# Performance work log

Measured on AMD Instinct MI355X. Metric: run time of the kernel, lower is better.

Reference implementation:

```python
import jax, jax.numpy as jnp
import numpy as np

B, N, F, C, L = 2, 2048, 64, 64, 4

def setup_inputs() -> dict:
    key = jax.random.key(0)
    k1, k2, k3, k4, k5 = jax.random.split(key, 5)
    V = jax.random.normal(k1, (B, N, F), dtype=jnp.float32)
    A = jax.random.uniform(k2, (B, N, N, L), dtype=jnp.float32)
    # xavier-normal-ish scale for w1; plain normals for w2/w3
    w1 = jax.random.normal(k3, (F, C), dtype=jnp.float32) * jnp.sqrt(2.0 / (F + C))
    w2 = jax.random.normal(k4, (F * L, C), dtype=jnp.float32) * 0.05
    w3 = jax.random.normal(k5, (F * L, C), dtype=jnp.float32) * 0.05
    return {"V": V, "A": A, "w1": w1, "w2": w2, "w3": w3}

def reference(V, A, w1, w2, w3):
    b, n, _, l = A.shape
    f = V.shape[-1]
    # term1: plain linear embedding (no bias, no act)
    term1 = jnp.matmul(V, w1)                                   # B,N,C
    # term2: per-edge-type degree weighting of self features
    deg = jnp.sum(A, axis=2)                                    # B,N,L  (sum over neighbors j)
    dv = (deg[..., None] * V[:, :, None, :]).reshape(b, n, l * f)  # B,N,L*F
    term2 = jnp.matmul(dv, w2)                                  # B,N,C
    # term3: neighbor aggregation per edge type
    agg = jnp.einsum('bijl,bjf->bilf', A, V).reshape(b, n, l * f)  # B,N,L*F
    term3 = jnp.matmul(agg, w3)                                 # B,N,C
    return jax.nn.sigmoid(term1 + term2 - term3)
```

## Files before the change

kernel.cpp:

```cpp
#include <hip/hip_runtime.h>

#define B_ 2
#define N_ 2048
#define F_ 64
#define C_ 64
#define L_ 4
#define SK 4
#define NJ (N_ / SK)
#define TSTEPS (NJ / 32)
#define PJ 40

typedef _Float16 half8 __attribute__((ext_vector_type(8)));
typedef _Float16 half2 __attribute__((ext_vector_type(2)));
typedef float floatx4 __attribute__((ext_vector_type(4)));

__global__ __launch_bounds__(256) void k0_transpose(const float* __restrict__ V,
                                                    _Float16* __restrict__ Vth) {
    __shared__ float tile[64][65];
    const int b  = blockIdx.x >> 5;
    const int j0 = (blockIdx.x & 31) * 64;
    const int tid = threadIdx.x;

    const floatx4* V4 = (const floatx4*)(V + ((size_t)(b * N_ + j0)) * F_);
#pragma unroll
    for (int s = 0; s < 4; ++s) {
        int g = tid + 256 * s;
        int jl = g >> 4;
        int fq = g & 15;
        floatx4 v = V4[jl * 16 + fq];
        tile[jl][fq * 4 + 0] = v.x;
        tile[jl][fq * 4 + 1] = v.y;
        tile[jl][fq * 4 + 2] = v.z;
        tile[jl][fq * 4 + 3] = v.w;
    }
    __syncthreads();

    const int f = tid >> 2;
    const int jb = (tid & 3) * 16;
    _Float16* dh = Vth + ((size_t)(b * F_ + f)) * N_ + j0 + jb;
#pragma unroll
    for (int u = 0; u < 16; u += 4) {
        half2 h01 = {(_Float16)tile[jb + u + 0][f], (_Float16)tile[jb + u + 1][f]};
        half2 h23 = {(_Float16)tile[jb + u + 2][f], (_Float16)tile[jb + u + 3][f]};
        *(half2*)(dh + u + 0) = h01;
        *(half2*)(dh + u + 2) = h23;
    }
}

__global__ __launch_bounds__(256, 4) void k1_agg(const float* __restrict__ A,
                                                 const _Float16* __restrict__ Vth,
                                                 float* __restrict__ aggT,
                                                 float* __restrict__ degT) {
    __shared__ _Float16 lds[2 * 4 * 16 * PJ];

    const int bid = blockIdx.x;
    const int b   = bid >> 9;
    const int rem = bid & 511;
    const int i0  = (rem >> 2) * 16;
    const int p   = rem & 3;
    const int tid  = threadIdx.x;
    const int w    = tid >> 6;
    const int lane = tid & 63;
    const int m    = lane & 15;
    const int q    = lane >> 4;

    const int i_s = tid >> 4;
    const int jp  = tid & 15;

    const floatx4* Abase = (const floatx4*)A + ((size_t)(b * N_ + i0 + i_s)) * N_ + p * NJ;
    const _Float16* Vrow = Vth + ((size_t)b * F_) * N_ + p * NJ;

    floatx4 acc0 = {0,0,0,0}, acc1 = {0,0,0,0}, acc2 = {0,0,0,0}, acc3 = {0,0,0,0};
    floatx4 accd = {0,0,0,0};

    half8 bones;
#pragma unroll
    for (int e = 0; e < 8; ++e) bones[e] = (m == 0) ? (_Float16)1.0f : (_Float16)0.0f;

    floatx4 a_cur0, a_cur1, a_nxt0, a_nxt1;
    half8 v_cur0, v_cur1, v_cur2, v_cur3, v_nxt0, v_nxt1, v_nxt2, v_nxt3;

#define LOAD_A(t, x0, x1) do { int jj = (t) * 32 + 2 * jp; x0 = Abase[jj]; x1 = Abase[jj + 1]; } while (0)
#define LOAD_V(t, v0, v1, v2, v3) do { int jj = (t) * 32 + q * 8;                                  \
        v0 = *(const half8*)(Vrow + (size_t)(0  + m) * N_ + jj);                                   \
        v1 = *(const half8*)(Vrow + (size_t)(16 + m) * N_ + jj);                                   \
        v2 = *(const half8*)(Vrow + (size_t)(32 + m) * N_ + jj);                                   \
        v3 = *(const half8*)(Vrow + (size_t)(48 + m) * N_ + jj); } while (0)

    LOAD_A(0, a_cur0, a_cur1);
    LOAD_V(0, v_cur0, v_cur1, v_cur2, v_cur3);
    LOAD_A(1, a_nxt0, a_nxt1);
    LOAD_V(1, v_nxt0, v_nxt1, v_nxt2, v_nxt3);

#pragma unroll 2
    for (int t = 0; t < TSTEPS; ++t) {
        const int buf = t & 1;
        _Float16* dst = lds + buf * (4 * 16 * PJ);
        {
            const float* c0 = (const float*)&a_cur0;
            const float* c1 = (const float*)&a_cur1;
#pragma unroll
            for (int l = 0; l < 4; ++l) {
                half2 h = {(_Float16)c0[l], (_Float16)c1[l]};
                *(half2*)(dst + (l * 16 + i_s) * PJ + 2 * jp) = h;
            }
        }
        __syncthreads();

        a_cur0 = a_nxt0; a_cur1 = a_nxt1;
        const int tn = (t + 2 < TSTEPS) ? (t + 2) : (TSTEPS - 1);
        LOAD_A(tn, a_nxt0, a_nxt1);

        half8 af = *(const half8*)(lds + buf * (4 * 16 * PJ) + (w * 16 + m) * PJ + q * 8);
        acc0 = __builtin_amdgcn_mfma_f32_16x16x32_f16(af, v_cur0, acc0, 0, 0, 0);
        acc1 = __builtin_amdgcn_mfma_f32_16x16x32_f16(af, v_cur1, acc1, 0, 0, 0);
        acc2 = __builtin_amdgcn_mfma_f32_16x16x32_f16(af, v_cur2, acc2, 0, 0, 0);
        acc3 = __builtin_amdgcn_mfma_f32_16x16x32_f16(af, v_cur3, acc3, 0, 0, 0);
        accd = __builtin_amdgcn_mfma_f32_16x16x32_f16(af, bones,  accd, 0, 0, 0);

        v_cur0 = v_nxt0; v_cur1 = v_nxt1; v_cur2 = v_nxt2; v_cur3 = v_nxt3;
        LOAD_V(tn, v_nxt0, v_nxt1, v_nxt2, v_nxt3);
    }
#undef LOAD_A
#undef LOAD_V

    float* aggb = aggT + ((size_t)(p * B_ + b)) * 256 * N_;
    const int ibase = i0 + q * 4;
    {
        int k = w * 64 + 0  + m; *(floatx4*)(aggb + (size_t)k * N_ + ibase) = acc0;
    }
    {
        int k = w * 64 + 16 + m; *(floatx4*)(aggb + (size_t)k * N_ + ibase) = acc1;
    }
    {
        int k = w * 64 + 32 + m; *(floatx4*)(aggb + (size_t)k * N_ + ibase) = acc2;
    }
    {
        int k = w * 64 + 48 + m; *(floatx4*)(aggb + (size_t)k * N_ + ibase) = acc3;
    }
    if (m == 0) {
        *(floatx4*)(degT + ((size_t)((p * B_ + b) * L_ + w)) * N_ + ibase) = accd;
    }
}

__global__ __launch_bounds__(256) void k2_out(const float* __restrict__ V,
                                              const float* __restrict__ degT,
                                              const float* __restrict__ aggT,
                                              const float* __restrict__ w1,
                                              const float* __restrict__ w2,
                                              const float* __restrict__ w3,
                                              float* __restrict__ out) {
    __shared__ float xsum[256][4];
    __shared__ float vt[4][64];
    __shared__ float dsum[4][4];

    const int raw = blockIdx.x;
    const int b   = raw >> 9;
    const int t9  = raw & 511;
    const int tile = ((t9 & 7) << 6) | (t9 >> 3);
    const int i0  = tile * 4;
    const int tid = threadIdx.x;

    {
        const int k = tid;
        const float* g = aggT + ((size_t)b * 256 + k) * N_ + i0;
        const size_t PS = (size_t)B_ * 256 * N_;
        floatx4 s = *(const floatx4*)(g);
        s += *(const floatx4*)(g + PS);
        s += *(const floatx4*)(g + 2 * PS);
        s += *(const floatx4*)(g + 3 * PS);
        *(floatx4*)&xsum[k][0] = s;
    }
    {
        const int il = tid >> 6, f = tid & 63;
        vt[il][f] = V[((size_t)(b * N_ + i0 + il)) * F_ + f];
    }
    if (tid < 16) {
        const int l = tid >> 2, il = tid & 3;
        float s = 0.0f;
#pragma unroll
        for (int p = 0; p < SK; ++p)
            s += degT[((size_t)((p * B_ + b) * L_ + l)) * N_ + i0 + il];
        dsum[l][il] = s;
    }
    __syncthreads();

    const int il = tid >> 6;
    const int c  = tid & 63;
    const float d0 = dsum[0][il], d1 = dsum[1][il], d2 = dsum[2][il], d3 = dsum[3][il];

    float acc = 0.0f;
#pragma unroll 4
    for (int f = 0; f < 64; ++f) {
        const float x = vt[il][f];
        acc += x        * w1[f * 64 + c];
        acc += (d0 * x) * w2[(0 * 64 + f) * 64 + c];
        acc += (d1 * x) * w2[(1 * 64 + f) * 64 + c];
        acc += (d2 * x) * w2[(2 * 64 + f) * 64 + c];
        acc += (d3 * x) * w2[(3 * 64 + f) * 64 + c];
    }
#pragma unroll 4
    for (int k = 0; k < 256; ++k) {
        acc -= xsum[k][il] * w3[k * 64 + c];
    }

    out[((size_t)(b * N_ + i0 + il)) * C_ + c] = 1.0f / (1.0f + __expf(-acc));
}

extern "C" void kernel_launch(void* const* d_in, const int* in_sizes, int n_in,
                              void* d_out, int out_size, void* d_ws, size_t ws_size,
                              hipStream_t stream) {
    const float* V  = (const float*)d_in[0];
    const float* A  = (const float*)d_in[1];
    const float* w1 = (const float*)d_in[2];
    const float* w2 = (const float*)d_in[3];
    const float* w3 = (const float*)d_in[4];
    float* out = (float*)d_out;

    char* ws = (char*)d_ws;
    float*    aggT = (float*)(ws);
    float*    degT = (float*)(ws + 16777216);
    _Float16* Vth  = (_Float16*)(ws + 17039360);

    hipLaunchKernelGGL(k0_transpose, dim3(B_ * (N_ / 64)), dim3(256), 0, stream, V, Vth);
    hipLaunchKernelGGL(k1_agg,       dim3(B_ * (N_ / 16) * SK), dim3(256), 0, stream,
                       A, Vth, aggT, degT);
    hipLaunchKernelGGL(k2_out,       dim3(B_ * (N_ / 4)), dim3(256), 0, stream,
                       V, degT, aggT, w1, w2, w3, out);
}
```

Baseline: 244.6 us.

## Reassociate weight projections before neighbor aggregation and reduce partials in-block

Precomputes U3 = V·w3 per edge type (fp16), U2 = V·w2 and T1 = V·w1 in the first kernel, so the A-aggregation multiplies A directly against projected features. The per-type results are summed across the four waves in LDS, so only a 64-wide partial per row goes out instead of the 256-wide aggT. This cuts workspace traffic and simplifies the final kernel to an elementwise combine plus sigmoid. The main A-streaming kernel keeps the same MFMA work, and the __syncthreads is swapped for an explicit waitcnt plus s_barrier. Holding U3 in fp16 may change rounding compared with holding V in fp16.

```diff
diff --git a/kernel.cpp b/kernel.cpp
--- a/kernel.cpp
+++ b/kernel.cpp
@@ -1,4 +1,5 @@
 #include <hip/hip_runtime.h>
+
 
 #define B_ 2
 #define N_ 2048
@@ -14,44 +15,70 @@
 typedef _Float16 half2 __attribute__((ext_vector_type(2)));
 typedef float floatx4 __attribute__((ext_vector_type(4)));
 
-__global__ __launch_bounds__(256) void k0_transpose(const float* __restrict__ V,
-                                                    _Float16* __restrict__ Vth) {
-    __shared__ float tile[64][65];
-    const int b  = blockIdx.x >> 5;
-    const int j0 = (blockIdx.x & 31) * 64;
+__global__ __launch_bounds__(256) void k0_embed(const float* __restrict__ V,
+                                                const float* __restrict__ w1,
+                                                const float* __restrict__ w2,
+                                                const float* __restrict__ w3,
+                                                _Float16* __restrict__ U3,
+                                                float* __restrict__ U2,
+                                                float* __restrict__ T1) {
+    __shared__ float vt[16][64];
+    const int b  = blockIdx.x >> 7;
+    const int j0 = (blockIdx.x & 127) * 16;
     const int tid = threadIdx.x;
 
-    const floatx4* V4 = (const floatx4*)(V + ((size_t)(b * N_ + j0)) * F_);
-#pragma unroll
-    for (int s = 0; s < 4; ++s) {
-        int g = tid + 256 * s;
-        int jl = g >> 4;
-        int fq = g & 15;
-        floatx4 v = V4[jl * 16 + fq];
-        tile[jl][fq * 4 + 0] = v.x;
-        tile[jl][fq * 4 + 1] = v.y;
-        tile[jl][fq * 4 + 2] = v.z;
-        tile[jl][fq * 4 + 3] = v.w;
+    {
+        const floatx4* Vv = (const floatx4*)(V + ((size_t)(b * N_ + j0)) * F_);
+        floatx4 v = Vv[tid];
+        *(floatx4*)&vt[tid >> 4][(tid & 15) * 4] = v;
     }
     __syncthreads();
 
-    const int f = tid >> 2;
-    const int jb = (tid & 3) * 16;
-    _Float16* dh = Vth + ((size_t)(b * F_ + f)) * N_ + j0 + jb;
-#pragma unroll
-    for (int u = 0; u < 16; u += 4) {
-        half2 h01 = {(_Float16)tile[jb + u + 0][f], (_Float16)tile[jb + u + 1][f]};
-        half2 h23 = {(_Float16)tile[jb + u + 2][f], (_Float16)tile[jb + u + 3][f]};
-        *(half2*)(dh + u + 0) = h01;
-        *(half2*)(dh + u + 2) = h23;
-    }
+    const int l = tid >> 6;
+    const int c = tid & 63;
+
+    float a3[16], a2[16];
+#pragma unroll
+    for (int r = 0; r < 16; ++r) { a3[r] = 0.0f; a2[r] = 0.0f; }
+    float a1[4] = {0.0f, 0.0f, 0.0f, 0.0f};
+
+#pragma unroll 4
+    for (int f = 0; f < 64; ++f) {
+        const float W3 = w3[(l * 64 + f) * 64 + c];
+        const float W2 = w2[(l * 64 + f) * 64 + c];
+        const float W1 = w1[f * 64 + c];
+#pragma unroll
+        for (int r = 0; r < 16; ++r) {
+            const float x = vt[r][f];
+            a3[r] += x * W3;
+            a2[r] += x * W2;
+        }
+#pragma unroll
+        for (int r = 0; r < 4; ++r) a1[r] += vt[l * 4 + r][f] * W1;
+    }
+
+    {
+        _Float16* du = U3 + (((size_t)b * 4 + l) * 64 + c) * N_ + j0;
+#pragma unroll
+        for (int r = 0; r < 16; r += 2) {
+            half2 h = {(_Float16)a3[r], (_Float16)a3[r + 1]};
+            *(half2*)(du + r) = h;
+        }
+    }
+#pragma unroll
+    for (int r = 0; r < 16; ++r)
+        U2[(((size_t)(b * N_ + j0 + r)) * 4 + l) * 64 + c] = a2[r];
+#pragma unroll
+    for (int r = 0; r < 4; ++r)
+        T1[((size_t)(b * N_ + j0 + l * 4 + r)) * 64 + c] = a1[r];
 }
 
 __global__ __launch_bounds__(256, 4) void k1_agg(const float* __restrict__ A,
-                                                 const _Float16* __restrict__ Vth,
-                                                 float* __restrict__ aggT,
+                                                 const _Float16* __restrict__ U3,
+                                                 float* __restrict__ Ppart,
                                                  float* __restrict__ degT) {
     __shared__ _Float16 lds[2 * 4 * 16 * PJ];
+    __shared__ float red[4][16][64];
 
     const int bid = blockIdx.x;
     const int b   = bid >> 9;
@@ -68,7 +95,7 @@
     const int jp  = tid & 15;
 
     const floatx4* Abase = (const floatx4*)A + ((size_t)(b * N_ + i0 + i_s)) * N_ + p * NJ;
-    const _Float16* Vrow = Vth + ((size_t)b * F_) * N_ + p * NJ;
+    const _Float16* Urow = U3 + (((size_t)b * 4 + w) * 64) * N_ + p * NJ;
 
     floatx4 acc0 = {0,0,0,0}, acc1 = {0,0,0,0}, acc2 = {0,0,0,0}, acc3 = {0,0,0,0};
     floatx4 accd = {0,0,0,0};
@@ -81,16 +108,16 @@
     half8 v_cur0, v_cur1, v_cur2, v_cur3, v_nxt0, v_nxt1, v_nxt2, v_nxt3;
 
 #define LOAD_A(t, x0, x1) do { int jj = (t) * 32 + 2 * jp; x0 = Abase[jj]; x1 = Abase[jj + 1]; } while (0)
-#define LOAD_V(t, v0, v1, v2, v3) do { int jj = (t) * 32 + q * 8;                                  \
-        v0 = *(const half8*)(Vrow + (size_t)(0  + m) * N_ + jj);                                   \
-        v1 = *(const half8*)(Vrow + (size_t)(16 + m) * N_ + jj);                                   \
-        v2 = *(const half8*)(Vrow + (size_t)(32 + m) * N_ + jj);                                   \
-        v3 = *(const half8*)(Vrow + (size_t)(48 + m) * N_ + jj); } while (0)
+#define LOAD_U(t, v0, v1, v2, v3) do { int jj = (t) * 32 + q * 8;                                  \
+        v0 = *(const half8*)(Urow + (size_t)(0  + m) * N_ + jj);                                   \
+        v1 = *(const half8*)(Urow + (size_t)(16 + m) * N_ + jj);                                   \
+        v2 = *(const half8*)(Urow + (size_t)(32 + m) * N_ + jj);                                   \
+        v3 = *(const half8*)(Urow + (size_t)(48 + m) * N_ + jj); } while (0)
 
     LOAD_A(0, a_cur0, a_cur1);
-    LOAD_V(0, v_cur0, v_cur1, v_cur2, v_cur3);
+    LOAD_U(0, v_cur0, v_cur1, v_cur2, v_cur3);
     LOAD_A(1, a_nxt0, a_nxt1);
-    LOAD_V(1, v_nxt0, v_nxt1, v_nxt2, v_nxt3);
+    LOAD_U(1, v_nxt0, v_nxt1, v_nxt2, v_nxt3);
 
 #pragma unroll 2
     for (int t = 0; t < TSTEPS; ++t) {
@@ -105,7 +132,10 @@
                 *(half2*)(dst + (l * 16 + i_s) * PJ + 2 * jp) = h;
             }
         }
-        __syncthreads();
+        __builtin_amdgcn_sched_barrier(0);
+        asm volatile("s_waitcnt lgkmcnt(0)" ::: "memory");
+        __builtin_amdgcn_s_barrier();
+        __builtin_amdgcn_sched_barrier(0);
 
         a_cur0 = a_nxt0; a_cur1 = a_nxt1;
         const int tn = (t + 2 < TSTEPS) ? (t + 2) : (TSTEPS - 1);
@@ -119,92 +149,77 @@
         accd = __builtin_amdgcn_mfma_f32_16x16x32_f16(af, bones,  accd, 0, 0, 0);
 
         v_cur0 = v_nxt0; v_cur1 = v_nxt1; v_cur2 = v_nxt2; v_cur3 = v_nxt3;
-        LOAD_V(tn, v_nxt0, v_nxt1, v_nxt2, v_nxt3);
+        LOAD_U(tn, v_nxt0, v_nxt1, v_nxt2, v_nxt3);
     }
 #undef LOAD_A
-#undef LOAD_V
-
-    float* aggb = aggT + ((size_t)(p * B_ + b)) * 256 * N_;
-    const int ibase = i0 + q * 4;
-    {
-        int k = w * 64 + 0  + m; *(floatx4*)(aggb + (size_t)k * N_ + ibase) = acc0;
-    }
-    {
-        int k = w * 64 + 16 + m; *(floatx4*)(aggb + (size_t)k * N_ + ibase) = acc1;
-    }
-    {
-        int k = w * 64 + 32 + m; *(floatx4*)(aggb + (size_t)k * N_ + ibase) = acc2;
-    }
-    {
-        int k = w * 64 + 48 + m; *(floatx4*)(aggb + (size_t)k * N_ + ibase) = acc3;
+#undef LOAD_U
+
+    {
+        const float* f0 = (const float*)&acc0;
+        const float* f1 = (const float*)&acc1;
+        const float* f2 = (const float*)&acc2;
+        const float* f3 = (const float*)&acc3;
+#pragma unroll
+        for (int r = 0; r < 4; ++r) {
+            red[w][q * 4 + r][ 0 + m] = f0[r];
+            red[w][q * 4 + r][16 + m] = f1[r];
+            red[w][q * 4 + r][32 + m] = f2[r];
+            red[w][q * 4 + r][48 + m] = f3[r];
+        }
     }
     if (m == 0) {
+        const int ibase = i0 + q * 4;
         *(floatx4*)(degT + ((size_t)((p * B_ + b) * L_ + w)) * N_ + ibase) = accd;
     }
-}
-
-__global__ __launch_bounds__(256) void k2_out(const float* __restrict__ V,
+    __syncthreads();
+
+    {
+        const int c = tid & 63;
+        float* Pb = Ppart + (((size_t)(p * B_ + b) * (N_ / 16) + (i0 >> 4)) * 16) * 64;
+#pragma unroll
+        for (int r = 0; r < 4; ++r) {
+            const int i = (tid >> 6) * 4 + r;
+            Pb[i * 64 + c] = red[0][i][c] + red[1][i][c] + red[2][i][c] + red[3][i][c];
+        }
+    }
+}
+
+__global__ __launch_bounds__(256) void k2_fin(const float* __restrict__ Ppart,
                                               const float* __restrict__ degT,
-                                              const float* __restrict__ aggT,
-                                              const float* __restrict__ w1,
-                                              const float* __restrict__ w2,
-                                              const float* __restrict__ w3,
+                                              const float* __restrict__ U2,
+                                              const float* __restrict__ T1,
                                               float* __restrict__ out) {
-    __shared__ float xsum[256][4];
-    __shared__ float vt[4][64];
-    __shared__ float dsum[4][4];
-
-    const int raw = blockIdx.x;
-    const int b   = raw >> 9;
-    const int t9  = raw & 511;
-    const int tile = ((t9 & 7) << 6) | (t9 >> 3);
-    const int i0  = tile * 4;
+    __shared__ float dsum[4][16];
+    const int b  = blockIdx.x >> 7;
+    const int i0 = (blockIdx.x & 127) * 16;
     const int tid = threadIdx.x;
 
-    {
-        const int k = tid;
-        const float* g = aggT + ((size_t)b * 256 + k) * N_ + i0;
-        const size_t PS = (size_t)B_ * 256 * N_;
-        floatx4 s = *(const floatx4*)(g);
-        s += *(const floatx4*)(g + PS);
-        s += *(const floatx4*)(g + 2 * PS);
-        s += *(const floatx4*)(g + 3 * PS);
-        *(floatx4*)&xsum[k][0] = s;
-    }
-    {
-        const int il = tid >> 6, f = tid & 63;
-        vt[il][f] = V[((size_t)(b * N_ + i0 + il)) * F_ + f];
-    }
-    if (tid < 16) {
-        const int l = tid >> 2, il = tid & 3;
+    if (tid < 64) {
+        const int l = tid >> 4, i = tid & 15;
         float s = 0.0f;
 #pragma unroll
         for (int p = 0; p < SK; ++p)
-            s += degT[((size_t)((p * B_ + b) * L_ + l)) * N_ + i0 + il];
-        dsum[l][il] = s;
+            s += degT[((size_t)((p * B_ + b) * L_ + l)) * N_ + i0 + i];
+        dsum[l][i] = s;
     }
     __syncthreads();
 
-    const int il = tid >> 6;
-    const int c  = tid & 63;
-    const float d0 = dsum[0][il], d1 = dsum[1][il], d2 = dsum[2][il], d3 = dsum[3][il];
-
-    float acc = 0.0f;
-#pragma unroll 4
-    for (int f = 0; f < 64; ++f) {
-        const float x = vt[il][f];
-        acc += x        * w1[f * 64 + c];
-        acc += (d0 * x) * w2[(0 * 64 + f) * 64 + c];
-        acc += (d1 * x) * w2[(1 * 64 + f) * 64 + c];
-        acc += (d2 * x) * w2[(2 * 64 + f) * 64 + c];
-        acc += (d3 * x) * w2[(3 * 64 + f) * 64 + c];
-    }
-#pragma unroll 4
-    for (int k = 0; k < 256; ++k) {
-        acc -= xsum[k][il] * w3[k * 64 + c];
-    }
-
-    out[((size_t)(b * N_ + i0 + il)) * C_ + c] = 1.0f / (1.0f + __expf(-acc));
+    const int g = tid >> 6, c = tid & 63;
+    const size_t PS = (size_t)B_ * (N_ / 16) * 16 * 64;
+    const float* Pb = Ppart + (((size_t)b * (N_ / 16) + (i0 >> 4)) * 16) * 64;
+
+#pragma unroll
+    for (int r = 0; r < 4; ++r) {
+        const int i = g * 4 + r;
+        const size_t row = (size_t)(b * N_ + i0 + i);
+        float acc = T1[row * 64 + c];
+        acc += dsum[0][i] * U2[(row * 4 + 0) * 64 + c];
+        acc += dsum[1][i] * U2[(row * 4 + 1) * 64 + c];
+        acc += dsum[2][i] * U2[(row * 4 + 2) * 64 + c];
+        acc += dsum[3][i] * U2[(row * 4 + 3) * 64 + c];
+        acc -= Pb[i * 64 + c] + Pb[PS + i * 64 + c] + Pb[2 * PS + i * 64 + c] + Pb[3 * PS + i * 64 + c];
+        out[row * 64 + c] = 1.0f / (1.0f + __expf(-acc));
+    }
 }
 
 extern "C" void kernel_launch(void* const* d_in, const int* in_sizes, int n_in,
@@ -218,13 +233,16 @@
     float* out = (float*)d_out;
 
     char* ws = (char*)d_ws;
-    float*    aggT = (float*)(ws);
-    float*    degT = (float*)(ws + 16777216);
-    _Float16* Vth  = (_Float16*)(ws + 17039360);
-
-    hipLaunchKernelGGL(k0_transpose, dim3(B_ * (N_ / 64)), dim3(256), 0, stream, V, Vth);
-    hipLaunchKernelGGL(k1_agg,       dim3(B_ * (N_ / 16) * SK), dim3(256), 0, stream,
-                       A, Vth, aggT, degT);
-    hipLaunchKernelGGL(k2_out,       dim3(B_ * (N_ / 4)), dim3(256), 0, stream,
-                       V, degT, aggT, w1, w2, w3, out);
-}
+    float*    Ppart = (float*)(ws);
+    float*    degT  = (float*)(ws + (4u << 20));
+    _Float16* U3    = (_Float16*)(ws + (4u << 20) + (256u << 10));
+    float*    U2    = (float*)(ws + (6u << 20) + (256u << 10));
+    float*    T1    = (float*)(ws + (10u << 20) + (256u << 10));
+
+    hipLaunchKernelGGL(k0_embed, dim3(B_ * (N_ / 16)), dim3(256), 0, stream,
+                       V, w1, w2, w3, U3, U2, T1);
+    hipLaunchKernelGGL(k1_agg,   dim3(B_ * (N_ / 16) * SK), dim3(256), 0, stream,
+                       A, U3, Ppart, degT);
+    hipLaunchKernelGGL(k2_fin,   dim3(B_ * (N_ / 16)), dim3(256), 0, stream,
+                       Ppart, degT, U2, T1, out);
+}
```

After: 256.9 us. 1.05x slower.
